# Performance work log

Hardware: AMD Instinct MI355X
Metric: run time of the kernel (lower is better)

## Reference

```python
import jax, jax.numpy as jnp
import numpy as np

B, CIN, COUT, K, H, W, PAD = 64, 64, 64, 3, 112, 112, 1

def setup_inputs() -> dict:
    key = jax.random.key(0)
    k1, k2, k3 = jax.random.split(key, 3)
    x_padded = jax.random.normal(k1, (B, CIN, H + 2 * PAD, W + 2 * PAD), dtype=jnp.float32)
    weight = jax.random.normal(k2, (COUT, CIN, K, K), dtype=jnp.float32) * 0.1
    bias = jax.random.normal(k3, (COUT,), dtype=jnp.float32)
    return {"x_padded": x_padded, "weight": weight, "bias": bias, "in_height": H, "in_width": W}

def reference(x_padded, weight, bias, in_height, in_width):
    # Faithful to source: inner channel loop OVERWRITES output, so only the
    # LAST input channel contributes. Input is already padded -> VALID conv.
    stride = 1
    x_last = x_padded[:, -1:, :, :]           # [B, 1, Hp, Wp]
    w_last = weight[:, -1:, :, :]             # [O, 1, K, K]
    out = jax.lax.conv_general_dilated(
        x_last, w_last,
        window_strides=(stride, stride),
        padding='VALID',
        dimension_numbers=('NCHW', 'OIHW', 'NCHW'))
    return out + bias[None, :, None, None]
```

## Files before the change

kernel.cpp:

```cpp
#include <hip/hip_runtime.h>


#define CB    64
#define CCIN  64
#define CCOUT 64
#define CH    112
#define CW    112
#define CHP   114
#define CWP   114
#define NCO   8
#define SPT   (CH * (CW/4))

typedef float v4f __attribute__((ext_vector_type(4)));

__global__ __launch_bounds__(256) void CustomConv2D_12953621365171_kernel(
    const float* __restrict__ x,
    const float* __restrict__ wt,
    const float* __restrict__ bias,
    float* __restrict__ out)
{
    int s = blockIdx.x * 256 + threadIdx.x;
    if (s >= SPT) return;
    const int co0 = blockIdx.y * NCO;
    const int b   = blockIdx.z;

    int h  = s / 28;
    int wv = s - h * 28;
    int w0 = wv * 4;

    const float* xs = x + ((size_t)b * CCIN + (CCIN - 1)) * (CHP * CWP);

    float r[3][6];
    #pragma unroll
    for (int kh = 0; kh < 3; ++kh) {
        const float* row = xs + (h + kh) * CWP + w0;
        __builtin_memcpy(&r[kh][0], row, 6 * sizeof(float));
    }

    #pragma unroll
    for (int j = 0; j < NCO; ++j) {
        const float* wp = wt + ((size_t)(co0 + j) * CCIN + (CCIN - 1)) * 9;
        float bv = bias[co0 + j];
        float a0 = bv, a1 = bv, a2 = bv, a3 = bv;
        #pragma unroll
        for (int kh = 0; kh < 3; ++kh) {
            float k0 = wp[kh * 3 + 0];
            float k1 = wp[kh * 3 + 1];
            float k2 = wp[kh * 3 + 2];
            float r0 = r[kh][0], r1 = r[kh][1], r2 = r[kh][2];
            float r3 = r[kh][3], r4 = r[kh][4], r5 = r[kh][5];
            a0 = fmaf(k0, r0, fmaf(k1, r1, fmaf(k2, r2, a0)));
            a1 = fmaf(k0, r1, fmaf(k1, r2, fmaf(k2, r3, a1)));
            a2 = fmaf(k0, r2, fmaf(k1, r3, fmaf(k2, r4, a2)));
            a3 = fmaf(k0, r3, fmaf(k1, r4, fmaf(k2, r5, a3)));
        }
        v4f o = { a0, a1, a2, a3 };
        size_t off = ((size_t)b * CCOUT + (co0 + j)) * (CH * CW) + (size_t)s * 4;
        __builtin_nontemporal_store(o, reinterpret_cast<v4f*>(out + off));
    }
}

extern "C" void kernel_launch(void* const* d_in, const int* in_sizes, int n_in,
                              void* d_out, int out_size, void* d_ws, size_t ws_size,
                              hipStream_t stream) {
    const float* x    = (const float*)d_in[0];
    const float* wt   = (const float*)d_in[1];
    const float* bias = (const float*)d_in[2];
    float* out = (float*)d_out;

    dim3 grid((SPT + 255) / 256,
              CCOUT / NCO,
              CB);
    dim3 block(256, 1, 1);

    CustomConv2D_12953621365171_kernel<<<grid, block, 0, stream>>>(x, wt, bias, out);
}
```

Measured before the change: 41.97 us.

## Assign one output channel per block and loop over spatial chunks per thread

Each block now handles a single output channel, with the weights and bias held in scalar registers. Each thread loops over four spatial chunks instead of computing eight output channels from one input patch. This swaps input reuse across channels for weight reuse across space. As a result the input reads grow roughly eightfold, relying on L2 to serve them, while output writes are spread over many more blocks. The kernel is store-bound at about 205MB of output, so the main effect is on the write pattern and occupancy.

```diff
diff --git a/kernel.cpp b/kernel.cpp
--- a/kernel.cpp
+++ b/kernel.cpp
@@ -8,8 +8,8 @@
 #define CW    112
 #define CHP   114
 #define CWP   114
-#define NCO   8
 #define SPT   (CH * (CW/4))
+#define JS    4
 
 typedef float v4f __attribute__((ext_vector_type(4)));
 
@@ -19,44 +19,51 @@
     const float* __restrict__ bias,
     float* __restrict__ out)
 {
-    int s = blockIdx.x * 256 + threadIdx.x;
-    if (s >= SPT) return;
-    const int co0 = blockIdx.y * NCO;
-    const int b   = blockIdx.z;
-
-    int h  = s / 28;
-    int wv = s - h * 28;
-    int w0 = wv * 4;
+    const int co = blockIdx.y;
+    const int b  = blockIdx.z;
+    const int s0 = blockIdx.x * (256 * JS) + threadIdx.x;
 
     const float* xs = x + ((size_t)b * CCIN + (CCIN - 1)) * (CHP * CWP);
+    const float* wp = wt + ((size_t)co * CCIN + (CCIN - 1)) * 9;
+    const float k00 = wp[0], k01 = wp[1], k02 = wp[2];
+    const float k10 = wp[3], k11 = wp[4], k12 = wp[5];
+    const float k20 = wp[6], k21 = wp[7], k22 = wp[8];
+    const float bv  = bias[co];
 
-    float r[3][6];
-    #pragma unroll
-    for (int kh = 0; kh < 3; ++kh) {
-        const float* row = xs + (h + kh) * CWP + w0;
-        __builtin_memcpy(&r[kh][0], row, 6 * sizeof(float));
-    }
+    float* op = out + ((size_t)b * CCOUT + co) * (CH * CW);
 
     #pragma unroll
-    for (int j = 0; j < NCO; ++j) {
-        const float* wp = wt + ((size_t)(co0 + j) * CCIN + (CCIN - 1)) * 9;
-        float bv = bias[co0 + j];
-        float a0 = bv, a1 = bv, a2 = bv, a3 = bv;
-        #pragma unroll
-        for (int kh = 0; kh < 3; ++kh) {
-            float k0 = wp[kh * 3 + 0];
-            float k1 = wp[kh * 3 + 1];
-            float k2 = wp[kh * 3 + 2];
-            float r0 = r[kh][0], r1 = r[kh][1], r2 = r[kh][2];
-            float r3 = r[kh][3], r4 = r[kh][4], r5 = r[kh][5];
-            a0 = fmaf(k0, r0, fmaf(k1, r1, fmaf(k2, r2, a0)));
-            a1 = fmaf(k0, r1, fmaf(k1, r2, fmaf(k2, r3, a1)));
-            a2 = fmaf(k0, r2, fmaf(k1, r3, fmaf(k2, r4, a2)));
-            a3 = fmaf(k0, r3, fmaf(k1, r4, fmaf(k2, r5, a3)));
+    for (int j = 0; j < JS; ++j) {
+        int s = s0 + j * 256;
+        if (s < SPT) {
+            int h  = s / 28;
+            int wv = s - h * 28;
+            int w0 = wv * 4;
+
+            float r[3][6];
+            #pragma unroll
+            for (int kh = 0; kh < 3; ++kh) {
+                const float* row = xs + (h + kh) * CWP + w0;
+                __builtin_memcpy(&r[kh][0], row, 6 * sizeof(float));
+            }
+
+            float a0 = bv, a1 = bv, a2 = bv, a3 = bv;
+            a0 = fmaf(k00, r[0][0], fmaf(k01, r[0][1], fmaf(k02, r[0][2], a0)));
+            a1 = fmaf(k00, r[0][1], fmaf(k01, r[0][2], fmaf(k02, r[0][3], a1)));
+            a2 = fmaf(k00, r[0][2], fmaf(k01, r[0][3], fmaf(k02, r[0][4], a2)));
+            a3 = fmaf(k00, r[0][3], fmaf(k01, r[0][4], fmaf(k02, r[0][5], a3)));
+            a0 = fmaf(k10, r[1][0], fmaf(k11, r[1][1], fmaf(k12, r[1][2], a0)));
+            a1 = fmaf(k10, r[1][1], fmaf(k11, r[1][2], fmaf(k12, r[1][3], a1)));
+            a2 = fmaf(k10, r[1][2], fmaf(k11, r[1][3], fmaf(k12, r[1][4], a2)));
+            a3 = fmaf(k10, r[1][3], fmaf(k11, r[1][4], fmaf(k12, r[1][5], a3)));
+            a0 = fmaf(k20, r[2][0], fmaf(k21, r[2][1], fmaf(k22, r[2][2], a0)));
+            a1 = fmaf(k20, r[2][1], fmaf(k21, r[2][2], fmaf(k22, r[2][3], a1)));
+            a2 = fmaf(k20, r[2][2], fmaf(k21, r[2][3], fmaf(k22, r[2][4], a2)));
+            a3 = fmaf(k20, r[2][3], fmaf(k21, r[2][4], fmaf(k22, r[2][5], a3)));
+
+            v4f o = { a0, a1, a2, a3 };
+            __builtin_nontemporal_store(o, reinterpret_cast<v4f*>(op + (size_t)s * 4));
         }
-        v4f o = { a0, a1, a2, a3 };
-        size_t off = ((size_t)b * CCOUT + (co0 + j)) * (CH * CW) + (size_t)s * 4;
-        __builtin_nontemporal_store(o, reinterpret_cast<v4f*>(out + off));
     }
 }
 
@@ -68,8 +75,8 @@
     const float* bias = (const float*)d_in[2];
     float* out = (float*)d_out;
 
-    dim3 grid((SPT + 255) / 256,
-              CCOUT / NCO,
+    dim3 grid((SPT + 256 * JS - 1) / (256 * JS),
+              CCOUT,
               CB);
     dim3 block(256, 1, 1);
 
```

Result: slower. 81.56 us (+94.3%).

## Stage input rows in LDS per block and halve output channels per block

Applied to the files above, without the earlier changes.

Each block now cooperatively loads the input rows it needs, covering the halo, into shared memory with vector loads. Threads then read their 3x6 windows from LDS instead of doing unaligned global loads. Output channels per block drop from 8 to 4, which doubles the grid and re-stages the input twice as often. The kernel is dominated by output writes, so the added sync and LDS traffic may not matter much.

```diff
diff --git a/kernel.cpp b/kernel.cpp
--- a/kernel.cpp
+++ b/kernel.cpp
@@ -8,10 +8,13 @@
 #define CW    112
 #define CHP   114
 #define CWP   114
-#define NCO   8
+#define NCO   4
 #define SPT   (CH * (CW/4))
+#define PLANE (CHP * CWP)
+#define LDSF  1504
 
 typedef float v4f __attribute__((ext_vector_type(4)));
+typedef float v2f __attribute__((ext_vector_type(2)));
 
 __global__ __launch_bounds__(256) void CustomConv2D_12953621365171_kernel(
     const float* __restrict__ x,
@@ -19,44 +22,68 @@
     const float* __restrict__ bias,
     float* __restrict__ out)
 {
-    int s = blockIdx.x * 256 + threadIdx.x;
-    if (s >= SPT) return;
+    __shared__ float lx[LDSF];
+
+    const int tid = threadIdx.x;
+    const int s0b = blockIdx.x * 256;
     const int co0 = blockIdx.y * NCO;
     const int b   = blockIdx.z;
 
-    int h  = s / 28;
-    int wv = s - h * 28;
-    int w0 = wv * 4;
+    const float* xs = x + ((size_t)b * CCIN + (CCIN - 1)) * PLANE;
 
-    const float* xs = x + ((size_t)b * CCIN + (CCIN - 1)) * (CHP * CWP);
+    const int hlo  = s0b / 28;
+    const int smax = min(SPT - 1, s0b + 255);
+    const int hmax = smax / 28;
+    const int off0 = (hlo * CWP) & ~3;
+    const int end  = (hmax + 3) * CWP;
+    const int len  = end - off0;
 
-    float r[3][6];
-    #pragma unroll
-    for (int kh = 0; kh < 3; ++kh) {
-        const float* row = xs + (h + kh) * CWP + w0;
-        __builtin_memcpy(&r[kh][0], row, 6 * sizeof(float));
+    for (int i = 4 * tid; i < len; i += 1024) {
+        if (off0 + i + 4 <= PLANE) {
+            *(v4f*)&lx[i] = *(const v4f*)&xs[off0 + i];
+        } else {
+            for (int k = 0; k < 4 && off0 + i + k < PLANE; ++k)
+                lx[i + k] = xs[off0 + i + k];
+        }
     }
+    __syncthreads();
 
-    #pragma unroll
-    for (int j = 0; j < NCO; ++j) {
-        const float* wp = wt + ((size_t)(co0 + j) * CCIN + (CCIN - 1)) * 9;
-        float bv = bias[co0 + j];
-        float a0 = bv, a1 = bv, a2 = bv, a3 = bv;
+    const int s = s0b + tid;
+    if (s < SPT) {
+        int h  = s / 28;
+        int wv = s - h * 28;
+        int w0 = wv * 4;
+
+        float r[3][6];
         #pragma unroll
         for (int kh = 0; kh < 3; ++kh) {
-            float k0 = wp[kh * 3 + 0];
-            float k1 = wp[kh * 3 + 1];
-            float k2 = wp[kh * 3 + 2];
-            float r0 = r[kh][0], r1 = r[kh][1], r2 = r[kh][2];
-            float r3 = r[kh][3], r4 = r[kh][4], r5 = r[kh][5];
-            a0 = fmaf(k0, r0, fmaf(k1, r1, fmaf(k2, r2, a0)));
-            a1 = fmaf(k0, r1, fmaf(k1, r2, fmaf(k2, r3, a1)));
-            a2 = fmaf(k0, r2, fmaf(k1, r3, fmaf(k2, r4, a2)));
-            a3 = fmaf(k0, r3, fmaf(k1, r4, fmaf(k2, r5, a3)));
+            int li = (h + kh) * CWP + w0 - off0;
+            v2f p0 = *(const v2f*)&lx[li];
+            v2f p1 = *(const v2f*)&lx[li + 2];
+            v2f p2 = *(const v2f*)&lx[li + 4];
+            r[kh][0] = p0.x; r[kh][1] = p0.y; r[kh][2] = p1.x;
+            r[kh][3] = p1.y; r[kh][4] = p2.x; r[kh][5] = p2.y;
         }
-        v4f o = { a0, a1, a2, a3 };
-        size_t off = ((size_t)b * CCOUT + (co0 + j)) * (CH * CW) + (size_t)s * 4;
-        __builtin_nontemporal_store(o, reinterpret_cast<v4f*>(out + off));
+
+        #pragma unroll
+        for (int j = 0; j < NCO; ++j) {
+            const float* wp = wt + ((size_t)(co0 + j) * CCIN + (CCIN - 1)) * 9;
+            float bv = bias[co0 + j];
+            float a0 = bv, a1 = bv, a2 = bv, a3 = bv;
+            #pragma unroll
+            for (int kh = 0; kh < 3; ++kh) {
+                float k0 = wp[kh * 3 + 0];
+                float k1 = wp[kh * 3 + 1];
+                float k2 = wp[kh * 3 + 2];
+                a0 = fmaf(k0, r[kh][0], fmaf(k1, r[kh][1], fmaf(k2, r[kh][2], a0)));
+                a1 = fmaf(k0, r[kh][1], fmaf(k1, r[kh][2], fmaf(k2, r[kh][3], a1)));
+                a2 = fmaf(k0, r[kh][2], fmaf(k1, r[kh][3], fmaf(k2, r[kh][4], a2)));
+                a3 = fmaf(k0, r[kh][3], fmaf(k1, r[kh][4], fmaf(k2, r[kh][5], a3)));
+            }
+            v4f o = { a0, a1, a2, a3 };
+            size_t off = ((size_t)b * CCOUT + (co0 + j)) * (CH * CW) + (size_t)s * 4;
+            __builtin_nontemporal_store(o, reinterpret_cast<v4f*>(out + off));
+        }
     }
 }
 
```

Result: no change. 42.18 us (+0.5%).
